# Performance work log

Measured on AMD Instinct MI355X. Metric: run time of the kernel, lower is better.

## Reference

```python
import jax, jax.numpy as jnp
import numpy as np

B, C, L, M, F, N = 4, 32, 256, 256, 8, 64  # N = L // 4 per build()


def setup_inputs() -> dict:
    key = jax.random.key(0)
    k1, k2, k3, k4 = jax.random.split(key, 4)
    return {
        "x_real": jax.random.normal(k1, (B, 1, C, L, M), dtype=jnp.float32),
        "x_imag": jax.random.normal(k2, (B, 1, C, L, M), dtype=jnp.float32),
        "w_real": jax.random.normal(k3, (F, C, N, 1), dtype=jnp.float32),
        "w_imag": jax.random.normal(k4, (F, C, N, 1), dtype=jnp.float32),
    }


def _interp_weights(w, L):
    """tfp.math.interp_regular_1d_grid along axis=-2: map x_targ=0..L-1 over
    ref range [0, L-1] onto an N-point regular grid, linear interpolation."""
    Nn = w.shape[-2]
    t = jnp.arange(L, dtype=jnp.float32) / (L - 1) * (Nn - 1)  # grid coords
    lo = jnp.clip(jnp.floor(t).astype(jnp.int32), 0, Nn - 2)
    frac = (t - lo.astype(jnp.float32))[:, None]               # (L, 1)
    return w[:, :, lo, :] * (1.0 - frac) + w[:, :, lo + 1, :] * frac  # (F,C,L,1)


def reference(x_real, x_imag, w_real, w_imag):
    Lm = x_real.shape[-2]
    wr = _interp_weights(w_real, Lm)  # (F, C, L, 1)
    wi = _interp_weights(w_imag, Lm)
    # complex multiply: (wr + i*wi) * (xr + i*xi), broadcast (B,1,C,L,M)->(B,F,C,L,M)
    pr = wr * x_real - wi * x_imag
    pi = wr * x_imag + wi * x_real
    scale = jnp.sqrt(1.0 + jnp.arange(Lm, dtype=jnp.float32))[:, None]  # self.l, (L,1)
    yr = jnp.mean(pr, axis=-3) * scale  # (B, F, L, M)
    yi = jnp.mean(pi, axis=-3) * scale
    yr = jax.nn.relu(yr)  # relu=True: relu applied to real part only
    return jnp.stack([yr, yi])  # (2, B, F, L, M) == (real, imag)
```

## Files before the change

### kernel.cpp

```cpp
#include <hip/hip_runtime.h>
#include <math.h>

constexpr int B_ = 4, C_ = 32, L_ = 256, M_ = 256, F_ = 8, N_ = 64;

__global__ __launch_bounds__(64) void sphereconv_kernel(
    const float* __restrict__ xr, const float* __restrict__ xi,
    const float* __restrict__ wr, const float* __restrict__ wi,
    float* __restrict__ out)
{
    __shared__ float ws[C_ * 16];

    const int b    = blockIdx.x >> 8;
    const int l    = blockIdx.x & (L_ - 1);
    const int lane = threadIdx.x;

    const float t = ((float)l / (float)(L_ - 1)) * (float)(N_ - 1);
    int lo = (int)floorf(t);
    if (lo > N_ - 2) lo = N_ - 2;
    const float frac = t - (float)lo;

#pragma unroll
    for (int i = 0; i < 8; ++i) {
        const int idx = lane * 8 + i;
        const int c   = idx >> 4;
        const int j   = idx & 15;
        const int f   = j & 7;
        const float* w = (j & 8) ? wi : wr;
        const int base = (f * C_ + c) * N_ + lo;
        ws[c * 16 + j] = w[base] * (1.0f - frac) + w[base + 1] * frac;
    }
    __syncthreads();

    float4 accr[F_], acci[F_];
#pragma unroll
    for (int f = 0; f < F_; ++f) {
        accr[f] = make_float4(0.f, 0.f, 0.f, 0.f);
        acci[f] = make_float4(0.f, 0.f, 0.f, 0.f);
    }

    const size_t strideC4 = (size_t)L_ * M_ / 4;
    const size_t xoff = ((size_t)b * C_) * L_ * M_ + (size_t)l * M_ + lane * 4;
    const float4* xr4 = (const float4*)(xr + xoff);
    const float4* xi4 = (const float4*)(xi + xoff);

#pragma unroll 4
    for (int c = 0; c < C_; ++c) {
        const float4 vr = xr4[c * strideC4];
        const float4 vi = xi4[c * strideC4];
        const float4 w0 = *(const float4*)&ws[c * 16 + 0];
        const float4 w1 = *(const float4*)&ws[c * 16 + 4];
        const float4 u0 = *(const float4*)&ws[c * 16 + 8];
        const float4 u1 = *(const float4*)&ws[c * 16 + 12];
        const float wrf[8] = {w0.x, w0.y, w0.z, w0.w, w1.x, w1.y, w1.z, w1.w};
        const float wif[8] = {u0.x, u0.y, u0.z, u0.w, u1.x, u1.y, u1.z, u1.w};
#pragma unroll
        for (int f = 0; f < F_; ++f) {
            const float a = wrf[f], bb = wif[f];
            accr[f].x += a * vr.x - bb * vi.x;  acci[f].x += a * vi.x + bb * vr.x;
            accr[f].y += a * vr.y - bb * vi.y;  acci[f].y += a * vi.y + bb * vr.y;
            accr[f].z += a * vr.z - bb * vi.z;  acci[f].z += a * vi.z + bb * vr.z;
            accr[f].w += a * vr.w - bb * vi.w;  acci[f].w += a * vi.w + bb * vr.w;
        }
    }

    const float scale = sqrtf(1.0f + (float)l) * (1.0f / (float)C_);
    const size_t o0      = (((size_t)b * F_) * L_ + l) * M_ + lane * 4;
    const size_t imagOff = (size_t)B_ * F_ * L_ * M_;
    const size_t fStride = (size_t)L_ * M_;
#pragma unroll
    for (int f = 0; f < F_; ++f) {
        float4 yr, yi;
        yr.x = fmaxf(accr[f].x * scale, 0.f);
        yr.y = fmaxf(accr[f].y * scale, 0.f);
        yr.z = fmaxf(accr[f].z * scale, 0.f);
        yr.w = fmaxf(accr[f].w * scale, 0.f);
        yi.x = acci[f].x * scale;
        yi.y = acci[f].y * scale;
        yi.z = acci[f].z * scale;
        yi.w = acci[f].w * scale;
        *(float4*)(out + o0 + (size_t)f * fStride)           = yr;
        *(float4*)(out + o0 + (size_t)f * fStride + imagOff) = yi;
    }
}

extern "C" void kernel_launch(void* const* d_in, const int* in_sizes, int n_in,
                              void* d_out, int out_size, void* d_ws, size_t ws_size,
                              hipStream_t stream) {
    const float* xr = (const float*)d_in[0];
    const float* xi = (const float*)d_in[1];
    const float* wr = (const float*)d_in[2];
    const float* wi = (const float*)d_in[3];
    float* out = (float*)d_out;
    sphereconv_kernel<<<dim3(B_ * L_), dim3(64), 0, stream>>>(xr, xi, wr, wi, out);
}
```

Measured before the change: 127.4 us.

## Split filters across four waves per block to raise occupancy

Each block now runs 256 threads as four waves, and each wave computes two of the eight filters instead of one wave computing all eight. This cuts per-thread accumulator registers from 64 to 16 and gives four times as many waves to hide the latency of memory loads. In exchange, each wave reloads the same x data, so x traffic depends on cache hits to avoid being multiplied.

```diff
diff --git a/kernel.cpp b/kernel.cpp
--- a/kernel.cpp
+++ b/kernel.cpp
@@ -3,7 +3,7 @@
 
 constexpr int B_ = 4, C_ = 32, L_ = 256, M_ = 256, F_ = 8, N_ = 64;
 
-__global__ __launch_bounds__(64) void sphereconv_kernel(
+__global__ __launch_bounds__(256, 4) void sphereconv_kernel(
     const float* __restrict__ xr, const float* __restrict__ xi,
     const float* __restrict__ wr, const float* __restrict__ wi,
     float* __restrict__ out)
@@ -12,75 +12,80 @@
 
     const int b    = blockIdx.x >> 8;
     const int l    = blockIdx.x & (L_ - 1);
-    const int lane = threadIdx.x;
+    const int tid  = threadIdx.x;
+    const int w    = tid >> 6;
+    const int lane = tid & 63;
 
-    const float t = ((float)l / (float)(L_ - 1)) * (float)(N_ - 1);
-    int lo = (int)floorf(t);
+    const float tc = ((float)l / (float)(L_ - 1)) * (float)(N_ - 1);
+    int lo = (int)floorf(tc);
     if (lo > N_ - 2) lo = N_ - 2;
-    const float frac = t - (float)lo;
+    const float frac = tc - (float)lo;
 
 #pragma unroll
-    for (int i = 0; i < 8; ++i) {
-        const int idx = lane * 8 + i;
-        const int c   = idx >> 4;
-        const int j   = idx & 15;
-        const int f   = j & 7;
-        const float* w = (j & 8) ? wi : wr;
+    for (int i = tid; i < C_ * 16; i += 256) {
+        const int c = i >> 4;
+        const int j = i & 15;
+        const int f = j & 7;
+        const float* wptr = (j & 8) ? wi : wr;
         const int base = (f * C_ + c) * N_ + lo;
-        ws[c * 16 + j] = w[base] * (1.0f - frac) + w[base + 1] * frac;
+        ws[c * 16 + j] = wptr[base] * (1.0f - frac) + wptr[base + 1] * frac;
     }
     __syncthreads();
-
-    float4 accr[F_], acci[F_];
-#pragma unroll
-    for (int f = 0; f < F_; ++f) {
-        accr[f] = make_float4(0.f, 0.f, 0.f, 0.f);
-        acci[f] = make_float4(0.f, 0.f, 0.f, 0.f);
-    }
 
     const size_t strideC4 = (size_t)L_ * M_ / 4;
     const size_t xoff = ((size_t)b * C_) * L_ * M_ + (size_t)l * M_ + lane * 4;
     const float4* xr4 = (const float4*)(xr + xoff);
     const float4* xi4 = (const float4*)(xi + xoff);
 
-#pragma unroll 4
+    float4 ar0 = {0,0,0,0}, ai0 = {0,0,0,0};
+    float4 ar1 = {0,0,0,0}, ai1 = {0,0,0,0};
+
+#pragma unroll 8
     for (int c = 0; c < C_; ++c) {
         const float4 vr = xr4[c * strideC4];
         const float4 vi = xi4[c * strideC4];
-        const float4 w0 = *(const float4*)&ws[c * 16 + 0];
-        const float4 w1 = *(const float4*)&ws[c * 16 + 4];
-        const float4 u0 = *(const float4*)&ws[c * 16 + 8];
-        const float4 u1 = *(const float4*)&ws[c * 16 + 12];
-        const float wrf[8] = {w0.x, w0.y, w0.z, w0.w, w1.x, w1.y, w1.z, w1.w};
-        const float wif[8] = {u0.x, u0.y, u0.z, u0.w, u1.x, u1.y, u1.z, u1.w};
-#pragma unroll
-        for (int f = 0; f < F_; ++f) {
-            const float a = wrf[f], bb = wif[f];
-            accr[f].x += a * vr.x - bb * vi.x;  acci[f].x += a * vi.x + bb * vr.x;
-            accr[f].y += a * vr.y - bb * vi.y;  acci[f].y += a * vi.y + bb * vr.y;
-            accr[f].z += a * vr.z - bb * vi.z;  acci[f].z += a * vi.z + bb * vr.z;
-            accr[f].w += a * vr.w - bb * vi.w;  acci[f].w += a * vi.w + bb * vr.w;
-        }
+        const float2 wrp = *(const float2*)&ws[c * 16 + 2 * w];
+        const float2 wip = *(const float2*)&ws[c * 16 + 8 + 2 * w];
+
+        ar0.x = fmaf(wrp.x, vr.x, fmaf(-wip.x, vi.x, ar0.x));
+        ar0.y = fmaf(wrp.x, vr.y, fmaf(-wip.x, vi.y, ar0.y));
+        ar0.z = fmaf(wrp.x, vr.z, fmaf(-wip.x, vi.z, ar0.z));
+        ar0.w = fmaf(wrp.x, vr.w, fmaf(-wip.x, vi.w, ar0.w));
+        ai0.x = fmaf(wrp.x, vi.x, fmaf( wip.x, vr.x, ai0.x));
+        ai0.y = fmaf(wrp.x, vi.y, fmaf( wip.x, vr.y, ai0.y));
+        ai0.z = fmaf(wrp.x, vi.z, fmaf( wip.x, vr.z, ai0.z));
+        ai0.w = fmaf(wrp.x, vi.w, fmaf( wip.x, vr.w, ai0.w));
+
+        ar1.x = fmaf(wrp.y, vr.x, fmaf(-wip.y, vi.x, ar1.x));
+        ar1.y = fmaf(wrp.y, vr.y, fmaf(-wip.y, vi.y, ar1.y));
+        ar1.z = fmaf(wrp.y, vr.z, fmaf(-wip.y, vi.z, ar1.z));
+        ar1.w = fmaf(wrp.y, vr.w, fmaf(-wip.y, vi.w, ar1.w));
+        ai1.x = fmaf(wrp.y, vi.x, fmaf( wip.y, vr.x, ai1.x));
+        ai1.y = fmaf(wrp.y, vi.y, fmaf( wip.y, vr.y, ai1.y));
+        ai1.z = fmaf(wrp.y, vi.z, fmaf( wip.y, vr.z, ai1.z));
+        ai1.w = fmaf(wrp.y, vi.w, fmaf( wip.y, vr.w, ai1.w));
     }
 
     const float scale = sqrtf(1.0f + (float)l) * (1.0f / (float)C_);
-    const size_t o0      = (((size_t)b * F_) * L_ + l) * M_ + lane * 4;
+    const int   f0      = 2 * w;
+    const size_t o0      = (((size_t)b * F_ + f0) * L_ + l) * M_ + lane * 4;
     const size_t imagOff = (size_t)B_ * F_ * L_ * M_;
     const size_t fStride = (size_t)L_ * M_;
-#pragma unroll
-    for (int f = 0; f < F_; ++f) {
-        float4 yr, yi;
-        yr.x = fmaxf(accr[f].x * scale, 0.f);
-        yr.y = fmaxf(accr[f].y * scale, 0.f);
-        yr.z = fmaxf(accr[f].z * scale, 0.f);
-        yr.w = fmaxf(accr[f].w * scale, 0.f);
-        yi.x = acci[f].x * scale;
-        yi.y = acci[f].y * scale;
-        yi.z = acci[f].z * scale;
-        yi.w = acci[f].w * scale;
-        *(float4*)(out + o0 + (size_t)f * fStride)           = yr;
-        *(float4*)(out + o0 + (size_t)f * fStride + imagOff) = yi;
-    }
+
+    float4 yr0, yi0, yr1, yi1;
+    yr0.x = fmaxf(ar0.x * scale, 0.f); yr0.y = fmaxf(ar0.y * scale, 0.f);
+    yr0.z = fmaxf(ar0.z * scale, 0.f); yr0.w = fmaxf(ar0.w * scale, 0.f);
+    yi0.x = ai0.x * scale; yi0.y = ai0.y * scale;
+    yi0.z = ai0.z * scale; yi0.w = ai0.w * scale;
+    yr1.x = fmaxf(ar1.x * scale, 0.f); yr1.y = fmaxf(ar1.y * scale, 0.f);
+    yr1.z = fmaxf(ar1.z * scale, 0.f); yr1.w = fmaxf(ar1.w * scale, 0.f);
+    yi1.x = ai1.x * scale; yi1.y = ai1.y * scale;
+    yi1.z = ai1.z * scale; yi1.w = ai1.w * scale;
+
+    *(float4*)(out + o0)                      = yr0;
+    *(float4*)(out + o0 + imagOff)            = yi0;
+    *(float4*)(out + o0 + fStride)            = yr1;
+    *(float4*)(out + o0 + fStride + imagOff)  = yi1;
 }
 
 extern "C" void kernel_launch(void* const* d_in, const int* in_sizes, int n_in,
@@ -91,5 +96,5 @@
     const float* wr = (const float*)d_in[2];
     const float* wi = (const float*)d_in[3];
     float* out = (float*)d_out;
-    sphereconv_kernel<<<dim3(B_ * L_), dim3(64), 0, stream>>>(xr, xi, wr, wi, out);
+    sphereconv_kernel<<<dim3(B_ * L_), dim3(256), 0, stream>>>(xr, xi, wr, wi, out);
 }
```

Measured after the change: 110.2 us. 1.16x faster.
